# Kernel optimization log

Measured on AMD Instinct MI355X. Metric: run time of the kernel, lower is better.

The kernel has to match this reference:

```python
import jax, jax.numpy as jnp
import numpy as np

N_NODES = 50000
N_EDGES = 800000


def setup_inputs() -> dict:
    key = jax.random.key(0)
    ks = jax.random.split(key, 8)
    feats = jax.random.normal(ks[0], (N_NODES, 256), dtype=jnp.float32)
    src = jax.random.randint(ks[1], (N_EDGES,), 0, N_NODES, dtype=jnp.int32)
    dst = jax.random.randint(ks[2], (N_EDGES,), 0, N_NODES, dtype=jnp.int32)
    # Glorot-ish init for GraphConv weights
    W0 = jax.random.normal(ks[3], (256, 256), dtype=jnp.float32) * (1.0 / 16.0)
    W1 = jax.random.normal(ks[4], (256, 256), dtype=jnp.float32) * (1.0 / 16.0)
    W2 = jax.random.normal(ks[5], (256, 128), dtype=jnp.float32) * (1.0 / 16.0)
    b0 = jnp.zeros((256,), dtype=jnp.float32)
    b1 = jnp.zeros((256,), dtype=jnp.float32)
    b2 = jnp.zeros((128,), dtype=jnp.float32)
    return {"feats": feats, "src": src, "dst": dst,
            "W0": W0, "b0": b0, "W1": W1, "b1": b1, "W2": W2, "b2": b2}


def _graph_conv(x, src, dst, W, b, activate):
    """DGL GraphConv with norm='both': h = D_in^{-1/2} A D_out^{-1/2} x W + b."""
    n = x.shape[0]
    e_ones = jnp.ones(src.shape[0], dtype=x.dtype)
    deg_out = jax.ops.segment_sum(e_ones, src, num_segments=n)  # out-degree (src norm)
    deg_in = jax.ops.segment_sum(e_ones, dst, num_segments=n)   # in-degree (dst norm)
    norm_src = jnp.where(deg_out > 0, deg_out, 1.0) ** -0.5
    norm_dst = jnp.where(deg_in > 0, deg_in, 1.0) ** -0.5
    h = x * norm_src[:, None]
    # transform first (in_feats >= out_feats path in DGL) then aggregate
    h = h @ W
    m = jax.ops.segment_sum(h[src], dst, num_segments=n)  # [N, out] neighbor sum
    h = m * norm_dst[:, None] + b
    if activate:
        h = jax.nn.relu(h)
    return h


def reference(feats, src, dst, W0, b0, W1, b1, W2, b2):
    # dropout is identity in eval mode
    h0 = _graph_conv(feats, src, dst, W0, b0, True)
    h1 = _graph_conv(h0, src, dst, W1, b1, True)
    h2 = _graph_conv(h1, src, dst, W2, b2, False)  # last layer: no activation
    return (h0, h1, h2, h2)  # (h_list..., h)
```

## Files before the change

kernel.cpp:

```cpp
#include <hip/hip_runtime.h>
#include <hip/hip_bf16.h>

#define NN 50000
#define NE 800000
#define MPAD 50048
#define BSTR 64

typedef __attribute__((ext_vector_type(8))) short short8;
typedef __attribute__((ext_vector_type(4))) float f32x4;
typedef __attribute__((ext_vector_type(4))) unsigned short us4;
typedef __attribute__((ext_vector_type(8))) unsigned short us8;

static __device__ __forceinline__ unsigned short f2bf(float f) {
    union { float f; unsigned int u; } v; v.f = f;
    unsigned int u = v.u;
    return (unsigned short)((u + 0x7FFFu + ((u >> 16) & 1u)) >> 16);
}
static __device__ __forceinline__ float bf2f(unsigned short h) {
    union { unsigned int u; float f; } v; v.u = ((unsigned int)h) << 16;
    return v.f;
}

__global__ void k_degsortW(const int* __restrict__ src, const int* __restrict__ dst,
                           int* __restrict__ degO, int* __restrict__ degI,
                           int* __restrict__ bucket,
                           const float* __restrict__ W0, const float* __restrict__ W1,
                           const float* __restrict__ W2,
                           unsigned short* __restrict__ W0T, unsigned short* __restrict__ W1T,
                           unsigned short* __restrict__ W2T) {
    int bid = blockIdx.x;
    int t = threadIdx.x;
    if (bid < NE / 256) {
        int e = bid * 256 + t;
        int s = src[e], d = dst[e];
        atomicAdd(&degO[s], 1);
        int p = atomicAdd(&degI[d], 1);
        bucket[d * BSTR + p] = s;
    } else {
        int i = (bid - NE / 256) * 256 + t;
        if (i < 65536) {
            int k = i >> 8, c = i & 255;
            W0T[c * 256 + k] = f2bf(W0[i]);
        } else if (i < 131072) {
            int j = i - 65536;
            int k = j >> 8, c = j & 255;
            W1T[c * 256 + k] = f2bf(W1[j]);
        } else {
            int j = i - 131072;
            int k = j >> 7, c = j & 127;
            W2T[c * 256 + k] = f2bf(W2[j]);
        }
    }
}

__global__ __launch_bounds__(256) void k_prep(const float* __restrict__ x,
                                              const int* __restrict__ degO,
                                              const int* __restrict__ degI,
                                              float* __restrict__ nS, float* __restrict__ nD,
                                              unsigned short* __restrict__ xb) {
    const int row = blockIdx.x * 4 + (threadIdx.x >> 6);
    const int l = threadIdx.x & 63;
    int o = degO[row];
    float ns = 1.0f / sqrtf((float)(o > 0 ? o : 1));
    if (l == 0) {
        int d = degI[row];
        nS[row] = ns;
        nD[row] = 1.0f / sqrtf((float)(d > 0 ? d : 1));
    }
    f32x4 v = *(const f32x4*)&x[(long)row * 256 + l * 4];
    us4 ob;
#pragma unroll
    for (int k = 0; k < 4; k++) ob[k] = f2bf(v[k] * ns);
    *(us4*)&xb[(long)row * 256 + l * 4] = ob;
}

__global__ __launch_bounds__(256) void k_aggb(const int* __restrict__ degI,
                                              const int* __restrict__ bucket,
                                              const unsigned short* __restrict__ xb,
                                              const float* __restrict__ nD,
                                              unsigned short* __restrict__ aggb) {
    const int node = blockIdx.x * 4 + (threadIdx.x >> 6);
    const int lane = threadIdx.x & 63;
    const int q = lane >> 4;
    const int cl = (lane & 15) * 16;
    if (node >= NN) {
        if (node < MPAD && q == 0) {
            us8 z = {0,0,0,0,0,0,0,0};
            *(us8*)&aggb[(long)node * 256 + cl] = z;
            *(us8*)&aggb[(long)node * 256 + cl + 8] = z;
        }
        return;
    }
    const int deg = degI[node];
    const int bidx = bucket[node * BSTR + lane];
    float acc[16];
#pragma unroll
    for (int k = 0; k < 16; k++) acc[k] = 0.f;
    int j = 0;
    for (; j + 8 <= deg; j += 8) {
        int s0 = __shfl(bidx, j + q, 64);
        int s1 = __shfl(bidx, j + 4 + q, 64);
        const unsigned short* g0 = &xb[(long)s0 * 256 + cl];
        const unsigned short* g1 = &xb[(long)s1 * 256 + cl];
        us8 a0 = *(const us8*)g0;
        us8 a1 = *(const us8*)(g0 + 8);
        us8 b0 = *(const us8*)g1;
        us8 b1 = *(const us8*)(g1 + 8);
#pragma unroll
        for (int k = 0; k < 8; k++) {
            acc[k]     += bf2f(a0[k]) + bf2f(b0[k]);
            acc[8 + k] += bf2f(a1[k]) + bf2f(b1[k]);
        }
    }
    if (j + 4 <= deg) {
        int s0 = __shfl(bidx, j + q, 64);
        const unsigned short* g0 = &xb[(long)s0 * 256 + cl];
        us8 a0 = *(const us8*)g0;
        us8 a1 = *(const us8*)(g0 + 8);
#pragma unroll
        for (int k = 0; k < 8; k++) { acc[k] += bf2f(a0[k]); acc[8 + k] += bf2f(a1[k]); }
        j += 4;
    }
    if (j < deg) {
        int s0 = __shfl(bidx, j + q, 64);
        if (q < deg - j) {
            const unsigned short* g0 = &xb[(long)s0 * 256 + cl];
            us8 a0 = *(const us8*)g0;
            us8 a1 = *(const us8*)(g0 + 8);
#pragma unroll
            for (int k = 0; k < 8; k++) { acc[k] += bf2f(a0[k]); acc[8 + k] += bf2f(a1[k]); }
        }
    }
#pragma unroll
    for (int k = 0; k < 16; k++) acc[k] += __shfl_xor(acc[k], 16, 64);
#pragma unroll
    for (int k = 0; k < 16; k++) acc[k] += __shfl_xor(acc[k], 32, 64);
    if (q == 0) {
        float nd = nD[node];
        us8 o0, o1;
#pragma unroll
        for (int k = 0; k < 8; k++) {
            o0[k] = f2bf(acc[k] * nd);
            o1[k] = f2bf(acc[8 + k] * nd);
        }
        *(us8*)&aggb[(long)node * 256 + cl] = o0;
        *(us8*)&aggb[(long)node * 256 + cl + 8] = o1;
    }
}

template<int NOUT, int MODE>
__global__ __launch_bounds__(256) void k_gemm(const unsigned short* __restrict__ A,
                                              const unsigned short* __restrict__ BT,
                                              const float* __restrict__ bias,
                                              const float* __restrict__ nS,
                                              float* __restrict__ outF,
                                              unsigned short* __restrict__ xbn,
                                              unsigned short* __restrict__ outB) {
    __shared__ unsigned short As[128][40];
    __shared__ unsigned short Bs[128][36];
    const int bm = blockIdx.x * 128;
    const int bn = blockIdx.y * 128;
    const int tid = threadIdx.x;
    const int lane = tid & 63;
    const int w = tid >> 6;
    const int wr = w >> 1, wc = w & 1;

    f32x4 acc[4][4];
#pragma unroll
    for (int m = 0; m < 4; m++)
#pragma unroll
        for (int n = 0; n < 4; n++) acc[m][n] = (f32x4){0.f, 0.f, 0.f, 0.f};

    for (int kt = 0; kt < 256; kt += 32) {
        {
            int r = tid >> 1, c = (tid & 1) * 16;
            const unsigned short* g = &A[(long)(bm + r) * 256 + kt + c];
            *(us8*)&As[r][c]     = *(const us8*)(g);
            *(us8*)&As[r][c + 8] = *(const us8*)(g + 8);
        }
        {
            int col = tid >> 1, kh = (tid & 1) * 16;
            const unsigned short* g = &BT[(long)(bn + col) * 256 + kt + kh];
            *(us8*)&Bs[col][kh]     = *(const us8*)(g);
            *(us8*)&Bs[col][kh + 8] = *(const us8*)(g + 8);
        }
        __syncthreads();

        union U { us4 h[2]; short8 s; };
        const int kb = (lane >> 4) * 4;
        short8 af[4], bf[4];
#pragma unroll
        for (int m = 0; m < 4; m++) {
            int r = wr * 64 + m * 16 + (lane & 15);
            U u; u.h[0] = *(const us4*)&As[r][kb]; u.h[1] = *(const us4*)&As[r][kb + 16];
            af[m] = u.s;
        }
#pragma unroll
        for (int n = 0; n < 4; n++) {
            int cl = wc * 64 + n * 16 + (lane & 15);
            U u; u.h[0] = *(const us4*)&Bs[cl][kb]; u.h[1] = *(const us4*)&Bs[cl][kb + 16];
            bf[n] = u.s;
        }
#pragma unroll
        for (int m = 0; m < 4; m++)
#pragma unroll
            for (int n = 0; n < 4; n++)
                acc[m][n] = __builtin_amdgcn_mfma_f32_16x16x32_bf16(af[m], bf[n], acc[m][n], 0, 0, 0);
        __syncthreads();
    }

#pragma unroll
    for (int m = 0; m < 4; m++) {
        int rbase = bm + wr * 64 + m * 16 + (lane >> 4) * 4;
        float ns[4];
        bool in[4];
        if (MODE == 0) {
#pragma unroll
            for (int j = 0; j < 4; j++) {
                int row = rbase + j;
                in[j] = row < NN;
                ns[j] = in[j] ? nS[row] : 0.f;
            }
        }
#pragma unroll
        for (int n = 0; n < 4; n++) {
            int gc = bn + wc * 64 + n * 16 + (lane & 15);
            float bb = (MODE == 0) ? bias[gc] : 0.f;
#pragma unroll
            for (int j = 0; j < 4; j++) {
                int row = rbase + j;
                if (MODE == 0) {
                    if (in[j]) {
                        float v = fmaxf(acc[m][n][j] + bb, 0.f);
                        __builtin_nontemporal_store(v, &outF[(long)row * 256 + gc]);
                        xbn[(long)row * 256 + gc] = f2bf(v * ns[j]);
                    } else {
                        xbn[(long)row * 256 + gc] = 0;
                    }
                } else {
                    outB[(long)row * NOUT + gc] = f2bf(acc[m][n][j]);
                }
            }
        }
    }
}

__global__ __launch_bounds__(256) void k_agg2(const int* __restrict__ degI,
                                              const int* __restrict__ bucket,
                                              const unsigned short* __restrict__ hgb,
                                              const float* __restrict__ nD,
                                              const float* __restrict__ b,
                                              float* __restrict__ h2,
                                              float* __restrict__ h2b) {
    const int node = blockIdx.x * 4 + (threadIdx.x >> 6);
    const int lane = threadIdx.x & 63;
    if (node >= NN) return;
    const int q = lane >> 4;
    const int cl = (lane & 15) * 8;
    const int deg = degI[node];
    const int bidx = bucket[node * BSTR + lane];
    float acc[8];
#pragma unroll
    for (int k = 0; k < 8; k++) acc[k] = 0.f;
    int j = 0;
    for (; j + 8 <= deg; j += 8) {
        int s0 = __shfl(bidx, j + q, 64);
        int s1 = __shfl(bidx, j + 4 + q, 64);
        us8 vA = *(const us8*)&hgb[(long)s0 * 128 + cl];
        us8 vB = *(const us8*)&hgb[(long)s1 * 128 + cl];
#pragma unroll
        for (int k = 0; k < 8; k++) acc[k] += bf2f(vA[k]) + bf2f(vB[k]);
    }
    if (j + 4 <= deg) {
        int s0 = __shfl(bidx, j + q, 64);
        us8 vA = *(const us8*)&hgb[(long)s0 * 128 + cl];
#pragma unroll
        for (int k = 0; k < 8; k++) acc[k] += bf2f(vA[k]);
        j += 4;
    }
    if (j < deg) {
        int s0 = __shfl(bidx, j + q, 64);
        if (q < deg - j) {
            us8 vA = *(const us8*)&hgb[(long)s0 * 128 + cl];
#pragma unroll
            for (int k = 0; k < 8; k++) acc[k] += bf2f(vA[k]);
        }
    }
#pragma unroll
    for (int k = 0; k < 8; k++) acc[k] += __shfl_xor(acc[k], 16, 64);
#pragma unroll
    for (int k = 0; k < 8; k++) acc[k] += __shfl_xor(acc[k], 32, 64);
    if (q == 0) {
        float nd = nD[node];
        f32x4 v0, v1;
#pragma unroll
        for (int k = 0; k < 4; k++) v0[k] = acc[k] * nd + b[cl + k];
#pragma unroll
        for (int k = 0; k < 4; k++) v1[k] = acc[4 + k] * nd + b[cl + 4 + k];
        __builtin_nontemporal_store(v0, (f32x4*)&h2[(long)node * 128 + cl]);
        __builtin_nontemporal_store(v1, (f32x4*)&h2[(long)node * 128 + cl + 4]);
        __builtin_nontemporal_store(v0, (f32x4*)&h2b[(long)node * 128 + cl]);
        __builtin_nontemporal_store(v1, (f32x4*)&h2b[(long)node * 128 + cl + 4]);
    }
}

extern "C" void kernel_launch(void* const* d_in, const int* in_sizes, int n_in,
                              void* d_out, int out_size, void* d_ws, size_t ws_size,
                              hipStream_t stream) {
    const float* feats = (const float*)d_in[0];
    const int*   src   = (const int*)d_in[1];
    const int*   dst   = (const int*)d_in[2];
    const float* W0 = (const float*)d_in[3];
    const float* b0 = (const float*)d_in[4];
    const float* W1 = (const float*)d_in[5];
    const float* b1 = (const float*)d_in[6];
    const float* W2 = (const float*)d_in[7];
    const float* b2 = (const float*)d_in[8];

    float* out = (float*)d_out;
    float* h0  = out;
    float* h1  = out + (long)NN * 256;
    float* h2  = out + 2L * NN * 256;
    float* h2b = out + 2L * NN * 256 + (long)NN * 128;

    char* ws = (char*)d_ws;
    size_t off = 0;
    auto alloc = [&](size_t bytes) { void* p = ws + off; off += (bytes + 255) & ~255UL; return p; };
    unsigned short* xb   = (unsigned short*)alloc((size_t)MPAD * 256 * 2);
    unsigned short* xb2  = (unsigned short*)alloc((size_t)MPAD * 256 * 2);
    unsigned short* aggb = (unsigned short*)alloc((size_t)MPAD * 256 * 2);
    unsigned short* hgb  = (unsigned short*)alloc((size_t)MPAD * 128 * 2);
    unsigned short* W0T = (unsigned short*)alloc(256 * 256 * 2);
    unsigned short* W1T = (unsigned short*)alloc(256 * 256 * 2);
    unsigned short* W2T = (unsigned short*)alloc(128 * 256 * 2);
    int*   zint   = (int*)alloc((size_t)2 * NN * 4);
    int*   degO   = zint;
    int*   degI   = zint + NN;
    float* nS     = (float*)alloc(NN * 4);
    float* nD     = (float*)alloc(NN * 4);
    int*   bucket = (int*)alloc((size_t)NN * BSTR * 4);

    hipMemsetAsync(zint, 0, (size_t)2 * NN * 4, stream);
    k_degsortW<<<NE / 256 + 640, 256, 0, stream>>>(src, dst, degO, degI, bucket,
                                                   W0, W1, W2, W0T, W1T, W2T);

    k_prep<<<NN / 4, 256, 0, stream>>>(feats, degO, degI, nS, nD, xb);

    k_aggb<<<MPAD / 4, 256, 0, stream>>>(degI, bucket, xb, nD, aggb);
    k_gemm<256, 0><<<dim3(MPAD / 128, 2), 256, 0, stream>>>(aggb, W0T, b0, nS, h0, xb2, nullptr);

    k_aggb<<<MPAD / 4, 256, 0, stream>>>(degI, bucket, xb2, nD, aggb);
    k_gemm<256, 0><<<dim3(MPAD / 128, 2), 256, 0, stream>>>(aggb, W1T, b1, nS, h1, xb, nullptr);

    k_gemm<128, 1><<<dim3(MPAD / 128, 1), 256, 0, stream>>>(xb, W2T, nullptr, nullptr, nullptr, nullptr, hgb);
    k_agg2<<<(NN + 3) / 4, 256, 0, stream>>>(degI, bucket, hgb, nD, b2, h2, h2b);
}
```

Before: 331.9 us.

## Split aggregation across column slices and store neighbor indices as 16-bit

```diff
diff --git a/kernel.cpp b/kernel.cpp
--- a/kernel.cpp
+++ b/kernel.cpp
@@ -23,7 +23,7 @@
 
 __global__ void k_degsortW(const int* __restrict__ src, const int* __restrict__ dst,
                            int* __restrict__ degO, int* __restrict__ degI,
-                           int* __restrict__ bucket,
+                           unsigned short* __restrict__ bucket,
                            const float* __restrict__ W0, const float* __restrict__ W1,
                            const float* __restrict__ W2,
                            unsigned short* __restrict__ W0T, unsigned short* __restrict__ W1T,
@@ -35,7 +35,7 @@
         int s = src[e], d = dst[e];
         atomicAdd(&degO[s], 1);
         int p = atomicAdd(&degI[d], 1);
-        bucket[d * BSTR + p] = s;
+        bucket[d * BSTR + p] = (unsigned short)s;
     } else {
         int i = (bid - NE / 256) * 256 + t;
         if (i < 65536) {
@@ -75,76 +75,59 @@
 }
 
 __global__ __launch_bounds__(256) void k_aggb(const int* __restrict__ degI,
-                                              const int* __restrict__ bucket,
+                                              const unsigned short* __restrict__ bucket,
                                               const unsigned short* __restrict__ xb,
                                               const float* __restrict__ nD,
                                               unsigned short* __restrict__ aggb) {
-    const int node = blockIdx.x * 4 + (threadIdx.x >> 6);
+    const int sl = blockIdx.x & 7;
+    const int node = (blockIdx.x >> 3) * 4 + (threadIdx.x >> 6);
     const int lane = threadIdx.x & 63;
-    const int q = lane >> 4;
-    const int cl = (lane & 15) * 16;
+    const int e = lane >> 3;
+    const int cl = sl * 32 + (lane & 7) * 4;
     if (node >= NN) {
-        if (node < MPAD && q == 0) {
-            us8 z = {0,0,0,0,0,0,0,0};
-            *(us8*)&aggb[(long)node * 256 + cl] = z;
-            *(us8*)&aggb[(long)node * 256 + cl + 8] = z;
-        }
+        if (node < MPAD && e == 0)
+            *(us4*)&aggb[(long)node * 256 + cl] = (us4){0, 0, 0, 0};
         return;
     }
     const int deg = degI[node];
-    const int bidx = bucket[node * BSTR + lane];
-    float acc[16];
-#pragma unroll
-    for (int k = 0; k < 16; k++) acc[k] = 0.f;
+    const int bidx = (int)bucket[node * BSTR + lane];
+    float acc[4] = {0.f, 0.f, 0.f, 0.f};
     int j = 0;
-    for (; j + 8 <= deg; j += 8) {
-        int s0 = __shfl(bidx, j + q, 64);
-        int s1 = __shfl(bidx, j + 4 + q, 64);
-        const unsigned short* g0 = &xb[(long)s0 * 256 + cl];
-        const unsigned short* g1 = &xb[(long)s1 * 256 + cl];
-        us8 a0 = *(const us8*)g0;
-        us8 a1 = *(const us8*)(g0 + 8);
-        us8 b0 = *(const us8*)g1;
-        us8 b1 = *(const us8*)(g1 + 8);
-#pragma unroll
-        for (int k = 0; k < 8; k++) {
-            acc[k]     += bf2f(a0[k]) + bf2f(b0[k]);
-            acc[8 + k] += bf2f(a1[k]) + bf2f(b1[k]);
-        }
-    }
-    if (j + 4 <= deg) {
-        int s0 = __shfl(bidx, j + q, 64);
-        const unsigned short* g0 = &xb[(long)s0 * 256 + cl];
-        us8 a0 = *(const us8*)g0;
-        us8 a1 = *(const us8*)(g0 + 8);
-#pragma unroll
-        for (int k = 0; k < 8; k++) { acc[k] += bf2f(a0[k]); acc[8 + k] += bf2f(a1[k]); }
-        j += 4;
+    for (; j + 16 <= deg; j += 16) {
+        int s0 = __shfl(bidx, j + e, 64);
+        int s1 = __shfl(bidx, j + 8 + e, 64);
+        us4 v0 = *(const us4*)&xb[(long)s0 * 256 + cl];
+        us4 v1 = *(const us4*)&xb[(long)s1 * 256 + cl];
+#pragma unroll
+        for (int k = 0; k < 4; k++) acc[k] += bf2f(v0[k]) + bf2f(v1[k]);
+    }
+    if (j + 8 <= deg) {
+        int s0 = __shfl(bidx, j + e, 64);
+        us4 v0 = *(const us4*)&xb[(long)s0 * 256 + cl];
+#pragma unroll
+        for (int k = 0; k < 4; k++) acc[k] += bf2f(v0[k]);
+        j += 8;
     }
     if (j < deg) {
-        int s0 = __shfl(bidx, j + q, 64);
-        if (q < deg - j) {
-            const unsigned short* g0 = &xb[(long)s0 * 256 + cl];
-            us8 a0 = *(const us8*)g0;
-            us8 a1 = *(const us8*)(g0 + 8);
-#pragma unroll
-            for (int k = 0; k < 8; k++) { acc[k] += bf2f(a0[k]); acc[8 + k] += bf2f(a1[k]); }
-        }
-    }
-#pragma unroll
-    for (int k = 0; k < 16; k++) acc[k] += __shfl_xor(acc[k], 16, 64);
-#pragma unroll
-    for (int k = 0; k < 16; k++) acc[k] += __shfl_xor(acc[k], 32, 64);
-    if (q == 0) {
+        int s0 = __shfl(bidx, j + e, 64);
+        if (e < deg - j) {
+            us4 v0 = *(const us4*)&xb[(long)s0 * 256 + cl];
+#pragma unroll
+            for (int k = 0; k < 4; k++) acc[k] += bf2f(v0[k]);
+        }
+    }
+#pragma unroll
+    for (int k = 0; k < 4; k++) acc[k] += __shfl_xor(acc[k], 8, 64);
+#pragma unroll
+    for (int k = 0; k < 4; k++) acc[k] += __shfl_xor(acc[k], 16, 64);
+#pragma unroll
+    for (int k = 0; k < 4; k++) acc[k] += __shfl_xor(acc[k], 32, 64);
+    if (e == 0) {
         float nd = nD[node];
-        us8 o0, o1;
-#pragma unroll
-        for (int k = 0; k < 8; k++) {
-            o0[k] = f2bf(acc[k] * nd);
-            o1[k] = f2bf(acc[8 + k] * nd);
-        }
-        *(us8*)&aggb[(long)node * 256 + cl] = o0;
-        *(us8*)&aggb[(long)node * 256 + cl + 8] = o1;
+        us4 o;
+#pragma unroll
+        for (int k = 0; k < 4; k++) o[k] = f2bf(acc[k] * nd);
+        *(us4*)&aggb[(long)node * 256 + cl] = o;
     }
 }
 
@@ -246,61 +229,60 @@
 }
 
 __global__ __launch_bounds__(256) void k_agg2(const int* __restrict__ degI,
-                                              const int* __restrict__ bucket,
+                                              const unsigned short* __restrict__ bucket,
                                               const unsigned short* __restrict__ hgb,
                                               const float* __restrict__ nD,
                                               const float* __restrict__ b,
                                               float* __restrict__ h2,
                                               float* __restrict__ h2b) {
-    const int node = blockIdx.x * 4 + (threadIdx.x >> 6);
+    const int sl = blockIdx.x & 7;
+    const int node = (blockIdx.x >> 3) * 4 + (threadIdx.x >> 6);
     const int lane = threadIdx.x & 63;
     if (node >= NN) return;
-    const int q = lane >> 4;
-    const int cl = (lane & 15) * 8;
+    const int e = lane >> 2;
+    const int cl = sl * 16 + (lane & 3) * 4;
     const int deg = degI[node];
-    const int bidx = bucket[node * BSTR + lane];
-    float acc[8];
-#pragma unroll
-    for (int k = 0; k < 8; k++) acc[k] = 0.f;
+    const int bidx = (int)bucket[node * BSTR + lane];
+    float acc[4] = {0.f, 0.f, 0.f, 0.f};
     int j = 0;
-    for (; j + 8 <= deg; j += 8) {
-        int s0 = __shfl(bidx, j + q, 64);
-        int s1 = __shfl(bidx, j + 4 + q, 64);
-        us8 vA = *(const us8*)&hgb[(long)s0 * 128 + cl];
-        us8 vB = *(const us8*)&hgb[(long)s1 * 128 + cl];
-#pragma unroll
-        for (int k = 0; k < 8; k++) acc[k] += bf2f(vA[k]) + bf2f(vB[k]);
-    }
-    if (j + 4 <= deg) {
-        int s0 = __shfl(bidx, j + q, 64);
-        us8 vA = *(const us8*)&hgb[(long)s0 * 128 + cl];
-#pragma unroll
-        for (int k = 0; k < 8; k++) acc[k] += bf2f(vA[k]);
-        j += 4;
+    for (; j + 32 <= deg; j += 32) {
+        int s0 = __shfl(bidx, j + e, 64);
+        int s1 = __shfl(bidx, j + 16 + e, 64);
+        us4 v0 = *(const us4*)&hgb[(long)s0 * 128 + cl];
+        us4 v1 = *(const us4*)&hgb[(long)s1 * 128 + cl];
+#pragma unroll
+        for (int k = 0; k < 4; k++) acc[k] += bf2f(v0[k]) + bf2f(v1[k]);
+    }
+    if (j + 16 <= deg) {
+        int s0 = __shfl(bidx, j + e, 64);
+        us4 v0 = *(const us4*)&hgb[(long)s0 * 128 + cl];
+#pragma unroll
+        for (int k = 0; k < 4; k++) acc[k] += bf2f(v0[k]);
+        j += 16;
     }
     if (j < deg) {
-        int s0 = __shfl(bidx, j + q, 64);
-        if (q < deg - j) {
-            us8 vA = *(const us8*)&hgb[(long)s0 * 128 + cl];
-#pragma unroll
-            for (int k = 0; k < 8; k++) acc[k] += bf2f(vA[k]);
-        }
-    }
-#pragma unroll
-    for (int k = 0; k < 8; k++) acc[k] += __shfl_xor(acc[k], 16, 64);
-#pragma unroll
-    for (int k = 0; k < 8; k++) acc[k] += __shfl_xor(acc[k], 32, 64);
-    if (q == 0) {
+        int s0 = __shfl(bidx, j + e, 64);
+        if (e < deg - j) {
+            us4 v0 = *(const us4*)&hgb[(long)s0 * 128 + cl];
+#pragma unroll
+            for (int k = 0; k < 4; k++) acc[k] += bf2f(v0[k]);
+        }
+    }
+#pragma unroll
+    for (int k = 0; k < 4; k++) acc[k] += __shfl_xor(acc[k], 4, 64);
+#pragma unroll
+    for (int k = 0; k < 4; k++) acc[k] += __shfl_xor(acc[k], 8, 64);
+#pragma unroll
+    for (int k = 0; k < 4; k++) acc[k] += __shfl_xor(acc[k], 16, 64);
+#pragma unroll
+    for (int k = 0; k < 4; k++) acc[k] += __shfl_xor(acc[k], 32, 64);
+    if (e == 0) {
         float nd = nD[node];
-        f32x4 v0, v1;
-#pragma unroll
-        for (int k = 0; k < 4; k++) v0[k] = acc[k] * nd + b[cl + k];
-#pragma unroll
-        for (int k = 0; k < 4; k++) v1[k] = acc[4 + k] * nd + b[cl + 4 + k];
-        __builtin_nontemporal_store(v0, (f32x4*)&h2[(long)node * 128 + cl]);
-        __builtin_nontemporal_store(v1, (f32x4*)&h2[(long)node * 128 + cl + 4]);
-        __builtin_nontemporal_store(v0, (f32x4*)&h2b[(long)node * 128 + cl]);
-        __builtin_nontemporal_store(v1, (f32x4*)&h2b[(long)node * 128 + cl + 4]);
+        f32x4 v;
+#pragma unroll
+        for (int k = 0; k < 4; k++) v[k] = acc[k] * nd + b[cl + k];
+        __builtin_nontemporal_store(v, (f32x4*)&h2[(long)node * 128 + cl]);
+        __builtin_nontemporal_store(v, (f32x4*)&h2b[(long)node * 128 + cl]);
     }
 }
 
@@ -338,7 +320,7 @@
     int*   degI   = zint + NN;
     float* nS     = (float*)alloc(NN * 4);
     float* nD     = (float*)alloc(NN * 4);
-    int*   bucket = (int*)alloc((size_t)NN * BSTR * 4);
+    unsigned short* bucket = (unsigned short*)alloc((size_t)NN * BSTR * 2);
 
     hipMemsetAsync(zint, 0, (size_t)2 * NN * 4, stream);
     k_degsortW<<<NE / 256 + 640, 256, 0, stream>>>(src, dst, degO, degI, bucket,
@@ -346,12 +328,12 @@
 
     k_prep<<<NN / 4, 256, 0, stream>>>(feats, degO, degI, nS, nD, xb);
 
-    k_aggb<<<MPAD / 4, 256, 0, stream>>>(degI, bucket, xb, nD, aggb);
+    k_aggb<<<8 * (MPAD / 4), 256, 0, stream>>>(degI, bucket, xb, nD, aggb);
     k_gemm<256, 0><<<dim3(MPAD / 128, 2), 256, 0, stream>>>(aggb, W0T, b0, nS, h0, xb2, nullptr);
 
-    k_aggb<<<MPAD / 4, 256, 0, stream>>>(degI, bucket, xb2, nD, aggb);
+    k_aggb<<<8 * (MPAD / 4), 256, 0, stream>>>(degI, bucket, xb2, nD, aggb);
     k_gemm<256, 0><<<dim3(MPAD / 128, 2), 256, 0, stream>>>(aggb, W1T, b1, nS, h1, xb, nullptr);
 
     k_gemm<128, 1><<<dim3(MPAD / 128, 1), 256, 0, stream>>>(xb, W2T, nullptr, nullptr, nullptr, nullptr, hgb);
-    k_agg2<<<(NN + 3) / 4, 256, 0, stream>>>(degI, bucket, hgb, nD, b2, h2, h2b);
-}
+    k_agg2<<<8 * ((NN + 3) / 4), 256, 0, stream>>>(degI, bucket, hgb, nD, b2, h2, h2b);
+}
```

After: 511.2 us. 54.0% more time.
